# Kernel tuning notes

Hardware: AMD Instinct MI355X
Metric: run time of the kernel (lower is better)

## Reference

```python
import jax, jax.numpy as jnp
import numpy as np

# Spherical-harmonics constants (from _need_const)
A0 = float(np.pi)
A1 = float(2 * np.pi / np.sqrt(3.0))
A2 = float(2 * np.pi / np.sqrt(8.0))
C0 = float(1 / np.sqrt(4 * np.pi))
C1 = float(np.sqrt(3.0) / np.sqrt(4 * np.pi))
C2 = float(3 * np.sqrt(5.0) / np.sqrt(12 * np.pi))
D0 = float(0.5 / np.sqrt(3.0))
# BlendParams defaults (pytorch3d)
SIGMA = 1e-4
GAMMA_B = 1e-4
BG = (1.0, 1.0, 1.0)
ZNEAR, ZFAR, EPS = 1.0, 100.0, 1e-10


def setup_inputs() -> dict:
    key = jax.random.key(0)
    ks = jax.random.split(key, 9)
    N, H, W, K, V, F = 4, 512, 512, 4, 36000, 70000
    texels = jax.random.uniform(ks[0], (N, H, W, K, 3), dtype=jnp.float32)
    b = jax.random.uniform(ks[1], (N, H, W, K, 3), dtype=jnp.float32) + 1e-3
    bary_coords = b / jnp.sum(b, axis=-1, keepdims=True)
    pix_to_face = jax.random.randint(ks[2], (N, H, W, K), -1, F)  # -1 = empty pixel
    zbuf = jax.random.uniform(ks[3], (N, H, W, K), minval=ZNEAR, maxval=ZFAR, dtype=jnp.float32)
    dists = jax.random.normal(ks[4], (N, H, W, K), dtype=jnp.float32) * 1e-4
    verts = jax.random.normal(ks[5], (V, 3), dtype=jnp.float32)
    faces = jax.random.randint(ks[6], (F, 3), 0, V)
    vn = jax.random.normal(ks[7], (V, 3), dtype=jnp.float32)
    vertex_normals = vn / jnp.linalg.norm(vn, axis=-1, keepdims=True)
    gamma = jax.random.normal(ks[8], (N, 27), dtype=jnp.float32) * 0.1
    return dict(texels=texels, bary_coords=bary_coords, zbuf=zbuf, dists=dists,
                verts=verts, vertex_normals=vertex_normals, gamma=gamma,
                pix_to_face=pix_to_face, faces=faces)


def _interp_face_attrs(pix_to_face, bary, attrs):
    # attrs: (F, 3, D); pix_to_face: (N,H,W,K); bary: (N,H,W,K,3)
    mask = (pix_to_face >= 0)
    idx = jnp.where(mask, pix_to_face, 0)
    g = attrs[idx]  # (N,H,W,K,3,D) gather
    out = jnp.einsum('nhwkv,nhwkvd->nhwkd', bary, g)
    return out * mask[..., None].astype(out.dtype)


def reference(texels, bary_coords, zbuf, dists, verts, vertex_normals, gamma, pix_to_face, faces):
    # flip x,y of vertex normals (as in phong_shading)
    vn = vertex_normals * jnp.asarray([-1.0, -1.0, 1.0], vertex_normals.dtype)
    faces_normals = vn[faces]  # (F,3,3)
    pixel_normals = _interp_face_attrs(pix_to_face, bary_coords, faces_normals)  # (N,H,W,K,3)
    # Note: pixel_coords (from verts) is computed in the original but unused since
    # lights/cameras/materials are None -> specular_color = 0.
    g = gamma.reshape(-1, 3, 9)
    g = g.at[:, :, 0].add(0.8)
    g = jnp.transpose(g, (0, 2, 1))  # (N,9,3)
    nx, ny, nz = pixel_normals[..., 0], pixel_normals[..., 1], pixel_normals[..., 2]
    Y = jnp.stack([
        jnp.full_like(nx, A0 * C0),
        -A1 * C1 * ny,
        A1 * C1 * nz,
        -A1 * C1 * nx,
        A2 * C2 * nx * ny,
        -A2 * C2 * ny * nz,
        A2 * C2 * D0 * (3.0 * nz * nz - 1.0),
        -A2 * C2 * nx * nz,
        A2 * C2 * 0.5 * (nx * nx - ny * ny),
    ], axis=-1)  # (N,H,W,K,9)
    lighting = jnp.einsum('nhwki,nij->nhwkj', Y, g)  # (N,H,W,K,3)
    colors = lighting * texels  # specular = 0
    # softmax_rgb_blend (pytorch3d)
    mask = (pix_to_face >= 0).astype(colors.dtype)
    prob = jax.nn.sigmoid(-dists / SIGMA) * mask
    alpha = 1.0 - jnp.prod(1.0 - prob, axis=-1)
    z_inv = (ZFAR - zbuf) / (ZFAR - ZNEAR) * mask
    z_inv_max = jnp.clip(jnp.max(z_inv, axis=-1, keepdims=True), EPS, None)
    w_num = prob * jnp.exp((z_inv - z_inv_max) / GAMMA_B)
    delta = jnp.clip(jnp.exp((EPS - z_inv_max) / GAMMA_B), EPS, None)
    denom = jnp.sum(w_num, axis=-1, keepdims=True) + delta
    weights = w_num / denom  # (N,H,W,K)
    rgb = jnp.einsum('nhwk,nhwkc->nhwc', weights, colors)
    bg = (delta / denom) * jnp.asarray(BG, colors.dtype)  # (N,H,W,3) via broadcast of (N,H,W,1)
    return jnp.concatenate([rgb + bg, alpha[..., None]], axis=-1)  # (N,H,W,4)
```

## Files before the change

### kernel.cpp

```cpp
#include <hip/hip_runtime.h>
#include <math.h>

#define C_A0 3.14159265358979323846f
#define C_A1 3.6275987284684357f
#define C_A2 2.2214414690791831f
#define C_C0 0.28209479177387814f
#define C_C1 0.48860251190291992f
#define C_C2 1.0925484305920792f
#define C_D0 0.28867513459481287f
#define C_SIGMA  1e-4f
#define C_GAMMAB 1e-4f
#define C_ZNEAR  1.0f
#define C_ZFAR   100.0f
#define C_EPS    1e-10f

__global__ __launch_bounds__(256) void build_face_table(
    const int* __restrict__ faces, const float* __restrict__ vn,
    float4* __restrict__ tbl, int F)
{
    int f = blockIdx.x * 256 + threadIdx.x;
    if (f >= F) return;
    float o[12];
#pragma unroll
    for (int v = 0; v < 3; ++v) {
        int vi = faces[f * 3 + v];
        o[v * 3 + 0] = -vn[vi * 3 + 0];
        o[v * 3 + 1] = -vn[vi * 3 + 1];
        o[v * 3 + 2] =  vn[vi * 3 + 2];
    }
    o[9] = o[10] = o[11] = 0.0f;
    float4* dst = tbl + (size_t)f * 3;
    dst[0] = make_float4(o[0], o[1], o[2],  o[3]);
    dst[1] = make_float4(o[4], o[5], o[6],  o[7]);
    dst[2] = make_float4(o[8], o[9], o[10], o[11]);
}

template <bool USE_TABLE>
__global__ __launch_bounds__(256) void shade_kernel(
    const float* __restrict__ texels,
    const float* __restrict__ bary,
    const float* __restrict__ zbuf,
    const float* __restrict__ dists,
    const float* __restrict__ vn,
    const float* __restrict__ gamma,
    const int*   __restrict__ p2f,
    const int*   __restrict__ faces,
    const float4* __restrict__ tbl,
    float4* __restrict__ out,
    int npix, int hw)
{
    int pix = blockIdx.x * 256 + threadIdx.x;
    if (pix >= npix) return;
    int n = (blockIdx.x * 256) / hw;
    const float* __restrict__ g = gamma + n * 27;

    int4   f4 = ((const int4*)p2f)[pix];
    float4 zb = ((const float4*)zbuf)[pix];
    float4 dd = ((const float4*)dists)[pix];

    float bl[12], tx[12];
    {
        const float4* bp = (const float4*)bary + (size_t)pix * 3;
        float4 b0 = bp[0], b1 = bp[1], b2 = bp[2];
        bl[0]=b0.x; bl[1]=b0.y; bl[2]=b0.z; bl[3]=b0.w;
        bl[4]=b1.x; bl[5]=b1.y; bl[6]=b1.z; bl[7]=b1.w;
        bl[8]=b2.x; bl[9]=b2.y; bl[10]=b2.z; bl[11]=b2.w;
        const float4* tp = (const float4*)texels + (size_t)pix * 3;
        float4 t0 = tp[0], t1 = tp[1], t2 = tp[2];
        tx[0]=t0.x; tx[1]=t0.y; tx[2]=t0.z; tx[3]=t0.w;
        tx[4]=t1.x; tx[5]=t1.y; tx[6]=t1.z; tx[7]=t1.w;
        tx[8]=t2.x; tx[9]=t2.y; tx[10]=t2.z; tx[11]=t2.w;
    }

    int   fidx[4] = { f4.x, f4.y, f4.z, f4.w };
    float zbv[4]  = { zb.x, zb.y, zb.z, zb.w };
    float ddv[4]  = { dd.x, dd.y, dd.z, dd.w };

    float prob[4], zinv[4], col[4][3];
    float zmax = C_EPS;

#pragma unroll
    for (int k = 0; k < 4; ++k) {
        int fc = fidx[k];
        float m = (fc >= 0) ? 1.0f : 0.0f;
        int fi = (fc >= 0) ? fc : 0;

        float w0 = bl[k * 3 + 0], w1 = bl[k * 3 + 1], w2 = bl[k * 3 + 2];
        float nx, ny, nz;
        if (USE_TABLE) {
            const float4* t = tbl + (size_t)fi * 3;
            float4 t0 = t[0], t1 = t[1], t2 = t[2];
            nx = w0 * t0.x + w1 * t0.w + w2 * t1.z;
            ny = w0 * t0.y + w1 * t1.x + w2 * t1.w;
            nz = w0 * t0.z + w1 * t1.y + w2 * t2.x;
        } else {
            nx = 0.0f; ny = 0.0f; nz = 0.0f;
#pragma unroll
            for (int v = 0; v < 3; ++v) {
                int vi = faces[fi * 3 + v];
                float w = bl[k * 3 + v];
                nx += w * (-vn[vi * 3 + 0]);
                ny += w * (-vn[vi * 3 + 1]);
                nz += w * ( vn[vi * 3 + 2]);
            }
        }
        nx *= m; ny *= m; nz *= m;

        float Yv[9];
        Yv[0] = C_A0 * C_C0;
        Yv[1] = -(C_A1 * C_C1) * ny;
        Yv[2] =  (C_A1 * C_C1) * nz;
        Yv[3] = -(C_A1 * C_C1) * nx;
        Yv[4] =  (C_A2 * C_C2) * nx * ny;
        Yv[5] = -(C_A2 * C_C2) * ny * nz;
        Yv[6] =  (C_A2 * C_C2) * C_D0 * (3.0f * nz * nz - 1.0f);
        Yv[7] = -(C_A2 * C_C2) * nx * nz;
        Yv[8] =  (C_A2 * C_C2) * 0.5f * (nx * nx - ny * ny);

#pragma unroll
        for (int c = 0; c < 3; ++c) {
            float l = Yv[0] * (g[c * 9 + 0] + 0.8f);
#pragma unroll
            for (int i = 1; i < 9; ++i) l += Yv[i] * g[c * 9 + i];
            col[k][c] = l * tx[k * 3 + c];
        }

        prob[k] = m / (1.0f + expf(ddv[k] / C_SIGMA));
        zinv[k] = (C_ZFAR - zbv[k]) / (C_ZFAR - C_ZNEAR) * m;
        zmax = fmaxf(zmax, zinv[k]);
    }

    float alpha = 1.0f - (1.0f - prob[0]) * (1.0f - prob[1])
                        * (1.0f - prob[2]) * (1.0f - prob[3]);

    float delta = expf((C_EPS - zmax) / C_GAMMAB);
    delta = fmaxf(delta, C_EPS);

    float wn[4];
    float denom = delta;
#pragma unroll
    for (int k = 0; k < 4; ++k) {
        wn[k] = prob[k] * expf((zinv[k] - zmax) / C_GAMMAB);
        denom += wn[k];
    }
    float inv = 1.0f / denom;

    float r = 0.0f, gc = 0.0f, b = 0.0f;
#pragma unroll
    for (int k = 0; k < 4; ++k) {
        r  += wn[k] * col[k][0];
        gc += wn[k] * col[k][1];
        b  += wn[k] * col[k][2];
    }
    r  = (r  + delta) * inv;
    gc = (gc + delta) * inv;
    b  = (b  + delta) * inv;

    out[pix] = make_float4(r, gc, b, alpha);
}

extern "C" void kernel_launch(void* const* d_in, const int* in_sizes, int n_in,
                              void* d_out, int out_size, void* d_ws, size_t ws_size,
                              hipStream_t stream) {
    const float* texels = (const float*)d_in[0];
    const float* bary   = (const float*)d_in[1];
    const float* zbuf   = (const float*)d_in[2];
    const float* dists  = (const float*)d_in[3];
    const float* vn     = (const float*)d_in[5];
    const float* gamma  = (const float*)d_in[6];
    const int*   p2f    = (const int*)d_in[7];
    const int*   faces  = (const int*)d_in[8];

    int nhwk = in_sizes[2];
    int npix = nhwk / 4;
    int N    = in_sizes[6] / 27;
    int hw   = npix / N;
    int F    = in_sizes[8] / 3;

    float4* out = (float4*)d_out;
    size_t tbl_bytes = (size_t)F * 12 * sizeof(float);

    int shade_blocks = (npix + 255) / 256;
    if (ws_size >= tbl_bytes) {
        float4* tbl = (float4*)d_ws;
        build_face_table<<<(F + 255) / 256, 256, 0, stream>>>(faces, vn, tbl, F);
        shade_kernel<true><<<shade_blocks, 256, 0, stream>>>(
            texels, bary, zbuf, dists, vn, gamma, p2f, faces, tbl, out, npix, hw);
    } else {
        shade_kernel<false><<<shade_blocks, 256, 0, stream>>>(
            texels, bary, zbuf, dists, vn, gamma, p2f, faces, nullptr, out, npix, hw);
    }
}
```

Baseline: 225.2 us.

## Quantize per-face normal table to 14-bit packed uint4 and prefetch gathers early

The per-face table of three flipped vertex normals is no longer stored as 48 bytes of float; it is quantized to nine 14-bit fixed-point values packed into one 16-byte uint4. The shading kernel now issues all four table gathers right after loading pix_to_face, so their latency overlaps the other streaming loads, and unpacks them in registers. This cuts gather traffic and cache footprint for the random face lookups. In exchange it adds bit-unpack ALU work and introduces about 1e-4 quantization error in the normals, which may or may not stay within tolerance.

```diff
diff --git a/kernel.cpp b/kernel.cpp
--- a/kernel.cpp
+++ b/kernel.cpp
@@ -16,23 +16,49 @@
 
 __global__ __launch_bounds__(256) void build_face_table(
     const int* __restrict__ faces, const float* __restrict__ vn,
-    float4* __restrict__ tbl, int F)
+    uint4* __restrict__ tbl, int F)
 {
     int f = blockIdx.x * 256 + threadIdx.x;
     if (f >= F) return;
-    float o[12];
+    float c[9];
 #pragma unroll
     for (int v = 0; v < 3; ++v) {
         int vi = faces[f * 3 + v];
-        o[v * 3 + 0] = -vn[vi * 3 + 0];
-        o[v * 3 + 1] = -vn[vi * 3 + 1];
-        o[v * 3 + 2] =  vn[vi * 3 + 2];
-    }
-    o[9] = o[10] = o[11] = 0.0f;
-    float4* dst = tbl + (size_t)f * 3;
-    dst[0] = make_float4(o[0], o[1], o[2],  o[3]);
-    dst[1] = make_float4(o[4], o[5], o[6],  o[7]);
-    dst[2] = make_float4(o[8], o[9], o[10], o[11]);
+        c[v * 3 + 0] = -vn[vi * 3 + 0];
+        c[v * 3 + 1] = -vn[vi * 3 + 1];
+        c[v * 3 + 2] =  vn[vi * 3 + 2];
+    }
+    unsigned long long lo = 0ull, hi = 0ull;
+#pragma unroll
+    for (int i = 0; i < 9; ++i) {
+        int q = (int)rintf(c[i] * 8191.0f);
+        q = q < -8191 ? -8191 : (q > 8191 ? 8191 : q);
+        unsigned long long u = (unsigned long long)(unsigned)(q + 8192) & 0x3FFFull;
+        int b = 14 * i;
+        if (b < 64) {
+            lo |= u << b;
+            if (b > 50) hi |= u >> (64 - b);
+        } else {
+            hi |= u << (b - 64);
+        }
+    }
+    tbl[f] = make_uint4((unsigned)lo, (unsigned)(lo >> 32),
+                        (unsigned)hi, (unsigned)(hi >> 32));
+}
+
+__device__ __forceinline__ void unpack9(uint4 q, float* __restrict__ c)
+{
+    unsigned long long lo = (unsigned long long)q.x | ((unsigned long long)q.y << 32);
+    unsigned long long hi = (unsigned long long)q.z | ((unsigned long long)q.w << 32);
+#pragma unroll
+    for (int i = 0; i < 9; ++i) {
+        int b = 14 * i;
+        unsigned v;
+        if (b <= 50)       v = (unsigned)(lo >> b) & 0x3FFFu;
+        else if (b == 56)  v = ((unsigned)(lo >> 56) | ((unsigned)hi << 8)) & 0x3FFFu;
+        else               v = (unsigned)(hi >> (b - 64)) & 0x3FFFu;
+        c[i] = (float)(int)v * (1.0f / 8191.0f) - (8192.0f / 8191.0f);
+    }
 }
 
 template <bool USE_TABLE>
@@ -45,7 +71,7 @@
     const float* __restrict__ gamma,
     const int*   __restrict__ p2f,
     const int*   __restrict__ faces,
-    const float4* __restrict__ tbl,
+    const uint4* __restrict__ tbl,
     float4* __restrict__ out,
     int npix, int hw)
 {
@@ -55,6 +81,15 @@
     const float* __restrict__ g = gamma + n * 27;
 
     int4   f4 = ((const int4*)p2f)[pix];
+    int    fidx[4] = { f4.x, f4.y, f4.z, f4.w };
+
+    uint4 qv[4];
+#pragma unroll
+    for (int k = 0; k < 4; ++k) {
+        int fi = fidx[k] >= 0 ? fidx[k] : 0;
+        if (USE_TABLE) qv[k] = tbl[fi];
+    }
+
     float4 zb = ((const float4*)zbuf)[pix];
     float4 dd = ((const float4*)dists)[pix];
 
@@ -72,7 +107,6 @@
         tx[8]=t2.x; tx[9]=t2.y; tx[10]=t2.z; tx[11]=t2.w;
     }
 
-    int   fidx[4] = { f4.x, f4.y, f4.z, f4.w };
     float zbv[4]  = { zb.x, zb.y, zb.z, zb.w };
     float ddv[4]  = { dd.x, dd.y, dd.z, dd.w };
 
@@ -88,11 +122,11 @@
         float w0 = bl[k * 3 + 0], w1 = bl[k * 3 + 1], w2 = bl[k * 3 + 2];
         float nx, ny, nz;
         if (USE_TABLE) {
-            const float4* t = tbl + (size_t)fi * 3;
-            float4 t0 = t[0], t1 = t[1], t2 = t[2];
-            nx = w0 * t0.x + w1 * t0.w + w2 * t1.z;
-            ny = w0 * t0.y + w1 * t1.x + w2 * t1.w;
-            nz = w0 * t0.z + w1 * t1.y + w2 * t2.x;
+            float c[9];
+            unpack9(qv[k], c);
+            nx = w0 * c[0] + w1 * c[3] + w2 * c[6];
+            ny = w0 * c[1] + w1 * c[4] + w2 * c[7];
+            nz = w0 * c[2] + w1 * c[5] + w2 * c[8];
         } else {
             nx = 0.0f; ny = 0.0f; nz = 0.0f;
 #pragma unroll
@@ -178,11 +212,11 @@
     int F    = in_sizes[8] / 3;
 
     float4* out = (float4*)d_out;
-    size_t tbl_bytes = (size_t)F * 12 * sizeof(float);
+    size_t tbl_bytes = (size_t)F * sizeof(uint4);
 
     int shade_blocks = (npix + 255) / 256;
     if (ws_size >= tbl_bytes) {
-        float4* tbl = (float4*)d_ws;
+        uint4* tbl = (uint4*)d_ws;
         build_face_table<<<(F + 255) / 256, 256, 0, stream>>>(faces, vn, tbl, F);
         shade_kernel<true><<<shade_blocks, 256, 0, stream>>>(
             texels, bary, zbuf, dists, vn, gamma, p2f, faces, tbl, out, npix, hw);
```

After: 196.4 us. 12.8% less time.
